# Performance work log

Hardware: AMD Instinct MI355X
Metric: run time of the kernel (lower is better)

Reference implementation:

```python
import jax, jax.numpy as jnp
import numpy as np

D_MODEL = 128
N_HEAD = 4
D_K = D_MODEL // N_HEAD
NEG = -1e30


def setup_inputs() -> dict:
    key = jax.random.key(0)
    ks = jax.random.split(key, 6)
    B, L = 8, 2048
    x = jax.random.normal(ks[0], (B, D_MODEL, L), dtype=jnp.float32)
    # mask: 1.0 = masked position (per mask_logits convention), 0.0 = keep
    mask = jax.random.randint(ks[1], (B, L), 0, 2).astype(jnp.float32)
    s = 1.0 / np.sqrt(D_MODEL)
    Wq = jax.random.normal(ks[2], (N_HEAD, D_MODEL, D_K), dtype=jnp.float32) * s
    Wk = jax.random.normal(ks[3], (N_HEAD, D_MODEL, D_K), dtype=jnp.float32) * s
    Wv = jax.random.normal(ks[4], (N_HEAD, D_MODEL, D_K), dtype=jnp.float32) * s
    Wo = jax.random.normal(ks[5], (D_MODEL, D_MODEL), dtype=jnp.float32) * s
    return {"x": x, "mask": mask, "Wq": Wq, "Wk": Wk, "Wv": Wv, "Wo": Wo}


def reference(x, mask, Wq, Wk, Wv, Wo):
    # x: [B, d_model, L] -> [B, L, d_model]
    xt = jnp.transpose(x, (0, 2, 1))
    # per-head projections, stacked over head axis: [B, H, L, d_k]
    q = jnp.einsum('bld,hdk->bhlk', xt, Wq)
    k = jnp.einsum('bld,hdk->bhlk', xt, Wk)
    v = jnp.einsum('bld,hdk->bhlk', xt, Wv)
    scale = 1.0 / jnp.sqrt(jnp.asarray(D_K, dtype=x.dtype))
    # scores: [B, H, Lq, Lk]
    scores = jnp.einsum('bhqd,bhkd->bhqk', q, k) * scale
    hmask = mask[:, None, None, :]  # additive pre-softmax mask over keys
    scores = scores * (1.0 - hmask) + hmask * NEG
    attn = jax.nn.softmax(scores, axis=-1)
    attn = attn * mask[:, None, :, None]  # multiplicative post-softmax mask over queries
    heads = jnp.einsum('bhqk,bhkd->bhqd', attn, v)  # [B, H, L, d_k]
    B, H, L, dk = heads.shape
    head = jnp.transpose(heads, (0, 2, 1, 3)).reshape(B, L, H * dk)  # concat heads
    out = head @ Wo  # [B, L, d_model]
    return jnp.transpose(out, (0, 2, 1))  # [B, d_model, L]
```

## Files before the change

kernel.cpp:

```cpp
#include <hip/hip_runtime.h>
#include <hip/hip_bf16.h>
#include <math.h>

#define BATCH 8
#define LSEQ 2048
#define DM 128
#define NH 4
#define DK 32

constexpr float SCALE = 0.17677669529663687f;
constexpr float LOG2E = 1.4426950408889634f;
constexpr float SL = SCALE * LOG2E;

typedef __attribute__((ext_vector_type(8))) __bf16 bf16x8;
typedef __attribute__((ext_vector_type(16))) float f32x16;
typedef __attribute__((ext_vector_type(2))) unsigned uint2v;

__device__ __forceinline__ bf16x8 as_bf16x8(uint4 u) {
    union { uint4 a; bf16x8 b; } c; c.a = u; return c.b;
}
__device__ __forceinline__ unsigned pack_bf2(float lo, float hi) {
    __hip_bfloat162 h = __float22bfloat162_rn(make_float2(lo, hi));
    union { __hip_bfloat162 a; unsigned b; } c; c.a = h; return c.b;
}
__device__ __forceinline__ unsigned short bf16u(float f) {
    union { __hip_bfloat16 h; unsigned short u; } c; c.h = __float2bfloat16(f); return c.u;
}

__global__ __launch_bounds__(256) void qkv_mfma_kernel(const float* __restrict__ x,
    const float* __restrict__ Wq, const float* __restrict__ Wk, const float* __restrict__ Wv,
    const float* __restrict__ mask,
    unsigned short* __restrict__ Qb, unsigned short* __restrict__ Kb,
    unsigned short* __restrict__ V4, int* __restrict__ cnt)
{
    const int b = blockIdx.x;
    const int which = blockIdx.y;
    const int lt = blockIdx.z;
    const int tid = threadIdx.x;
    const int wv = tid >> 6;
    const int lane = tid & 63;
    const int ql = lane & 31;
    const int hi = lane >> 5;
    const int l = lt * 64 + (wv & 1) * 32 + ql;
    const int hbase = (wv >> 1) * 2;

    __shared__ unsigned short wl[4][16][32][8];
    __shared__ int slotbuf[64];
    __shared__ int wsumI[4];

    const float* W = (which == 0 ? Wq : (which == 1 ? Wk : Wv));

    #pragma unroll
    for (int it = 0; it < 16; ++it) {
        const int flat = (it * 256 + tid) * 4;
        float4 v = *reinterpret_cast<const float4*>(W + flat);
        const int dk0 = flat & 31;
        const int d   = (flat >> 5) & 127;
        const int h   = flat >> 12;
        wl[h][d >> 3][dk0 + 0][d & 7] = bf16u(v.x);
        wl[h][d >> 3][dk0 + 1][d & 7] = bf16u(v.y);
        wl[h][d >> 3][dk0 + 2][d & 7] = bf16u(v.z);
        wl[h][d >> 3][dk0 + 3][d & 7] = bf16u(v.w);
    }

    if (which != 0) {
        const int nchunk = (lt + 1) * 8;
        int c = 0;
        if (tid < nchunk) {
            const float* mb = mask + (size_t)b * LSEQ + tid * 8;
            #pragma unroll
            for (int i = 0; i < 8; ++i) c += (mb[i] == 0.0f) ? 1 : 0;
        }
        int inc = c;
        #pragma unroll
        for (int off = 1; off < 64; off <<= 1) {
            int v = __shfl_up(inc, off);
            if (lane >= off) inc += v;
        }
        if (lane == 63) wsumI[wv] = inc;
        __syncthreads();
        int wpre = 0;
        #pragma unroll
        for (int wN = 0; wN < 4; ++wN) if (wN < wv) wpre += wsumI[wN];
        const int excl = wpre + inc - c;
        if (tid >= lt * 8 && tid < lt * 8 + 8) {
            const float* mb = mask + (size_t)b * LSEQ + tid * 8;
            int run = excl;
            #pragma unroll
            for (int i = 0; i < 8; ++i) {
                slotbuf[(tid - lt * 8) * 8 + i] = run;
                run += (mb[i] == 0.0f) ? 1 : 0;
            }
        }
        if (which == 1 && lt == 31 && tid == 255) cnt[b] = wpre + inc;
    }
    __syncthreads();

    const float* xcol = x + (size_t)b * DM * LSEQ + l;

    f32x16 acc0, acc1;
    #pragma unroll
    for (int r = 0; r < 16; ++r) { acc0[r] = 0.f; acc1[r] = 0.f; }

    #pragma unroll
    for (int d0 = 0; d0 < DM; d0 += 16) {
        const int dblk = (d0 >> 3) + hi;
        float xv[8];
        #pragma unroll
        for (int i = 0; i < 8; ++i) xv[i] = xcol[(size_t)(d0 + 8 * hi + i) * LSEQ];
        uint4 xp = make_uint4(pack_bf2(xv[0], xv[1]), pack_bf2(xv[2], xv[3]),
                              pack_bf2(xv[4], xv[5]), pack_bf2(xv[6], xv[7]));
        const bf16x8 xf = as_bf16x8(xp);
        uint4 wp0 = *reinterpret_cast<const uint4*>(&wl[hbase + 0][dblk][ql][0]);
        uint4 wp1 = *reinterpret_cast<const uint4*>(&wl[hbase + 1][dblk][ql][0]);
        acc0 = __builtin_amdgcn_mfma_f32_32x32x16_bf16(as_bf16x8(wp0), xf, acc0, 0, 0, 0);
        acc1 = __builtin_amdgcn_mfma_f32_32x32x16_bf16(as_bf16x8(wp1), xf, acc1, 0, 0, 0);
    }

    bool store = true;
    int slot = l;
    if (which != 0) {
        if (mask[(size_t)b * LSEQ + l] == 0.0f) slot = slotbuf[(wv & 1) * 32 + ql];
        else store = false;
    }
    if (store) {
        if (which < 2) {
            const float fold = (which == 0) ? SL : 1.0f;
            unsigned short* base0 = (which == 0 ? Qb : Kb);
            #pragma unroll
            for (int hh = 0; hh < 2; ++hh) {
                const f32x16& A = hh ? acc1 : acc0;
                const int bh = b * NH + hbase + hh;
                unsigned short* rowp = base0 + ((size_t)bh * LSEQ + slot) * DK;
                unsigned dw[8];
                #pragma unroll
                for (int j = 0; j < 8; ++j) dw[j] = pack_bf2(A[2*j] * fold, A[2*j+1] * fold);
                *reinterpret_cast<uint2*>(rowp + 4*hi)      = make_uint2(dw[0], dw[1]);
                *reinterpret_cast<uint2*>(rowp + 8 + 4*hi)  = make_uint2(dw[2], dw[3]);
                *reinterpret_cast<uint2*>(rowp + 16 + 4*hi) = make_uint2(dw[4], dw[5]);
                *reinterpret_cast<uint2*>(rowp + 24 + 4*hi) = make_uint2(dw[6], dw[7]);
            }
        } else {
            const int sbase = (slot >> 5) * 1024 + ((slot >> 4) & 1) * 512
                            + ((slot >> 3) & 1) * 256 + (slot & 7) + hi * 32;
            #pragma unroll
            for (int hh = 0; hh < 2; ++hh) {
                const f32x16& A = hh ? acc1 : acc0;
                const int bh = b * NH + hbase + hh;
                unsigned short* vb = V4 + (size_t)bh * (LSEQ * DK) + sbase;
                #pragma unroll
                for (int r = 0; r < 16; ++r)
                    vb[8 * (r & 3) + 64 * (r >> 2)] = bf16u(A[r]);
            }
        }
    }
}

__global__ __launch_bounds__(512, 4) void attnproj_kernel(
    const unsigned short* __restrict__ Qb, const unsigned short* __restrict__ Kb,
    const unsigned short* __restrict__ V4, const float* __restrict__ mask,
    const int* __restrict__ cnt, const float* __restrict__ Wo,
    float* __restrict__ out)
{
    const int b = blockIdx.x & 7;
    const int q0 = (blockIdx.x >> 3) * 32;
    const int tid = threadIdx.x;
    const int wid = tid >> 6;
    const int h = wid >> 1;
    const int kw = wid & 1;
    const int lane = tid & 63;
    const int ql = lane & 31;
    const int hi = lane >> 5;
    const int bh = b * NH + h;
    const int n = cnt[b];

    __shared__ __align__(16) char smem[17408];
    float* red = reinterpret_cast<float*>(smem);
    unsigned short* hd = reinterpret_cast<unsigned short*>(smem);

    const uint4* Qp = reinterpret_cast<const uint4*>(Qb + ((size_t)bh * LSEQ + q0 + ql) * DK);
    const bf16x8 qf0 = as_bf16x8(Qp[hi]);
    const bf16x8 qf1 = as_bf16x8(Qp[2 + hi]);

    const unsigned short* Kbase = Kb + (size_t)bh * LSEQ * DK;
    const unsigned short* Vb4   = V4 + (size_t)bh * LSEQ * DK;

    f32x16 acc;
    #pragma unroll
    for (int r = 0; r < 16; ++r) acc[r] = 0.f;
    f32x16 zero;
    #pragma unroll
    for (int r = 0; r < 16; ++r) zero[r] = 0.f;
    float la0 = 0.f, la1 = 0.f;

    auto ldk0 = [&](int k) { return reinterpret_cast<const uint4*>(Kbase + (size_t)(k + ql) * DK)[hi]; };
    auto ldk1 = [&](int k) { return reinterpret_cast<const uint4*>(Kbase + (size_t)(k + ql) * DK)[2 + hi]; };
    auto ldv0 = [&](int k) { return reinterpret_cast<const uint4*>(Vb4 + (size_t)(k >> 5) * 1024)[lane]; };
    auto ldv1 = [&](int k) { return reinterpret_cast<const uint4*>(Vb4 + (size_t)(k >> 5) * 1024)[64 + lane]; };

    auto compute = [&](uint4 kv0, uint4 kv1, uint4 vv0, uint4 vv1, int k0, bool pred) {
        f32x16 s = __builtin_amdgcn_mfma_f32_32x32x16_bf16(as_bf16x8(kv0), qf0, zero, 0, 0, 0);
        s = __builtin_amdgcn_mfma_f32_32x32x16_bf16(as_bf16x8(kv1), qf1, s, 0, 0, 0);
        unsigned w[8];
        #pragma unroll
        for (int j = 0; j < 8; ++j) {
            float e0 = exp2f(s[2*j]);
            float e1 = exp2f(s[2*j+1]);
            if (pred) {
                const int r0 = 2*j, r1 = 2*j + 1;
                if (k0 + (r0 & 3) + 8*(r0 >> 2) + 4*hi >= n) e0 = 0.f;
                if (k0 + (r1 & 3) + 8*(r1 >> 2) + 4*hi >= n) e1 = 0.f;
            }
            la0 += e0;
            la1 += e1;
            w[j] = pack_bf2(e0, e1);
        }
        uint2v p0 = __builtin_amdgcn_permlane32_swap(w[0], w[2], false, false);
        uint2v p1 = __builtin_amdgcn_permlane32_swap(w[1], w[3], false, false);
        uint2v p2 = __builtin_amdgcn_permlane32_swap(w[4], w[6], false, false);
        uint2v p3 = __builtin_amdgcn_permlane32_swap(w[5], w[7], false, false);
        uint4 b0 = make_uint4(p0[0], p1[0], p0[1], p1[1]);
        uint4 b1 = make_uint4(p2[0], p3[0], p2[1], p3[1]);
        acc = __builtin_amdgcn_mfma_f32_32x32x16_bf16(as_bf16x8(vv0), as_bf16x8(b0), acc, 0, 0, 0);
        acc = __builtin_amdgcn_mfma_f32_32x32x16_bf16(as_bf16x8(vv1), as_bf16x8(b1), acc, 0, 0, 0);
    };

    const int nfull = n & ~31;
    int k = kw * 32;
    if (k < nfull) {
        uint4 ka0 = ldk0(k), ka1 = ldk1(k), va0 = ldv0(k), va1 = ldv1(k);
        for (; k + 64 < nfull; k += 64) {
            uint4 kb0 = ldk0(k + 64), kb1 = ldk1(k + 64);
            uint4 vb0 = ldv0(k + 64), vb1 = ldv1(k + 64);
            compute(ka0, ka1, va0, va1, k, false);
            ka0 = kb0; ka1 = kb1; va0 = vb0; va1 = vb1;
        }
        compute(ka0, ka1, va0, va1, k, false);
    }
    if ((n & 31) && (((nfull >> 5) & 1) == kw)) {
        uint4 ka0 = ldk0(nfull), ka1 = ldk1(nfull);
        uint4 va0 = ldv0(nfull), va1 = ldv1(nfull);
        compute(ka0, ka1, va0, va1, nfull, true);
    }

    float la = la0 + la1;

    if (kw == 1) {
        float* r0 = red + ((size_t)h * 64 + lane) * 17;
        #pragma unroll
        for (int r = 0; r < 16; ++r) r0[r] = acc[r];
        r0[16] = la;
    }
    __syncthreads();
    float wgt = 0.f;
    if (kw == 0) {
        const float* r0 = red + ((size_t)h * 64 + lane) * 17;
        #pragma unroll
        for (int r = 0; r < 16; ++r) acc[r] += r0[r];
        la += r0[16];
        const float lf = la + __shfl_xor(la, 32);
        const float mq = mask[(size_t)b * LSEQ + q0 + ql];
        wgt = (lf > 0.f) ? (mq / lf) : 0.f;
    }
    __syncthreads();

    if (kw == 0) {
        unsigned short* hrow = hd + ql * 136 + h * DK + 4 * hi;
        #pragma unroll
        for (int g = 0; g < 4; ++g) {
            uint2 p = make_uint2(pack_bf2(acc[4*g+0]*wgt, acc[4*g+1]*wgt),
                                 pack_bf2(acc[4*g+2]*wgt, acc[4*g+3]*wgt));
            *reinterpret_cast<uint2*>(hrow + 8*g) = p;
        }
    }
    __syncthreads();

    if (wid < 4) {
        const int jq = wid;
        f32x16 pacc;
        #pragma unroll
        for (int r = 0; r < 16; ++r) pacc[r] = 0.f;
        #pragma unroll
        for (int ks = 0; ks < 8; ++ks) {
            const int k0 = ks * 16 + 8 * hi;
            uint4 bp = *reinterpret_cast<const uint4*>(hd + ql * 136 + k0);
            const float* wcol = Wo + (size_t)k0 * DM + jq * 32 + ql;
            float w[8];
            #pragma unroll
            for (int i = 0; i < 8; ++i) w[i] = wcol[(size_t)i * DM];
            uint4 ap = make_uint4(pack_bf2(w[0], w[1]), pack_bf2(w[2], w[3]),
                                  pack_bf2(w[4], w[5]), pack_bf2(w[6], w[7]));
            pacc = __builtin_amdgcn_mfma_f32_32x32x16_bf16(as_bf16x8(ap), as_bf16x8(bp), pacc, 0, 0, 0);
        }
        float* obase = out + (size_t)b * DM * LSEQ + q0 + ql;
        #pragma unroll
        for (int r = 0; r < 16; ++r) {
            const int j = jq * 32 + (r & 3) + 8 * (r >> 2) + 4 * hi;
            obase[(size_t)j * LSEQ] = pacc[r];
        }
    }
}

extern "C" void kernel_launch(void* const* d_in, const int* in_sizes, int n_in,
                              void* d_out, int out_size, void* d_ws, size_t ws_size,
                              hipStream_t stream)
{
    const float* x    = (const float*)d_in[0];
    const float* mask = (const float*)d_in[1];
    const float* Wq   = (const float*)d_in[2];
    const float* Wk   = (const float*)d_in[3];
    const float* Wv   = (const float*)d_in[4];
    const float* Wo   = (const float*)d_in[5];
    float* out = (float*)d_out;

    char* wsb = (char*)d_ws;
    const size_t NBF = (size_t)BATCH * NH * LSEQ * DK;
    unsigned short* Qb  = (unsigned short*)wsb;
    unsigned short* Kb  = Qb + NBF;
    unsigned short* V4  = Kb + NBF;
    int* cnt  = (int*)(wsb + 24ull * 1024 * 1024);

    qkv_mfma_kernel<<<dim3(BATCH, 3, LSEQ / 64), dim3(256), 0, stream>>>(
        x, Wq, Wk, Wv, mask, Qb, Kb, V4, cnt);
    attnproj_kernel<<<dim3(BATCH * LSEQ / 32), dim3(512), 0, stream>>>(
        Qb, Kb, V4, mask, cnt, Wo, out);
}
```

Baseline: 43.35 us.

## Compact masked-out queries and skip attention for them

The QKV kernel now also compacts query rows, storing only queries whose post-softmax mask is nonzero, and records scatter index lists for kept and dropped positions. The attention kernel processes only the compacted queries; blocks past the kept count just write zeros to the dropped output columns. This removes attention and projection work for query rows that the multiplicative mask zeroes anyway. In exchange, output stores become scattered through index lists, there is extra index-list traffic, and the saving depends on how many queries the mask drops.

After: 42.32 us. 2.4% less time.

```diff
diff --git a/kernel.cpp b/kernel.cpp
--- a/kernel.cpp
+++ b/kernel.cpp
@@ -31,7 +31,8 @@
     const float* __restrict__ Wq, const float* __restrict__ Wk, const float* __restrict__ Wv,
     const float* __restrict__ mask,
     unsigned short* __restrict__ Qb, unsigned short* __restrict__ Kb,
-    unsigned short* __restrict__ V4, int* __restrict__ cnt)
+    unsigned short* __restrict__ V4, int* __restrict__ cnt,
+    int* __restrict__ qpos1, int* __restrict__ qpos0)
 {
     const int b = blockIdx.x;
     const int which = blockIdx.y;
@@ -63,7 +64,7 @@
         wl[h][d >> 3][dk0 + 3][d & 7] = bf16u(v.w);
     }
 
-    if (which != 0) {
+    {
         const int nchunk = (lt + 1) * 8;
         int c = 0;
         if (tid < nchunk) {
@@ -95,6 +96,13 @@
         if (which == 1 && lt == 31 && tid == 255) cnt[b] = wpre + inc;
     }
     __syncthreads();
+
+    if (which == 1 && tid < 64) {
+        const int l64 = lt * 64 + tid;
+        const int s = slotbuf[tid];
+        if (mask[(size_t)b * LSEQ + l64] == 0.0f) qpos0[b * LSEQ + s] = l64;
+        else                                      qpos1[b * LSEQ + (l64 - s)] = l64;
+    }
 
     const float* xcol = x + (size_t)b * DM * LSEQ + l;
 
@@ -117,12 +125,12 @@
         acc1 = __builtin_amdgcn_mfma_f32_32x32x16_bf16(as_bf16x8(wp1), xf, acc1, 0, 0, 0);
     }
 
-    bool store = true;
-    int slot = l;
-    if (which != 0) {
-        if (mask[(size_t)b * LSEQ + l] == 0.0f) slot = slotbuf[(wv & 1) * 32 + ql];
-        else store = false;
-    }
+    const float mv = mask[(size_t)b * LSEQ + l];
+    const int zb = slotbuf[(wv & 1) * 32 + ql];
+    bool store;
+    int slot;
+    if (which == 0) { store = (mv != 0.0f); slot = l - zb; }
+    else            { store = (mv == 0.0f); slot = zb; }
     if (store) {
         if (which < 2) {
             const float fold = (which == 0) ? SL : 1.0f;
@@ -158,8 +166,9 @@
 
 __global__ __launch_bounds__(512, 4) void attnproj_kernel(
     const unsigned short* __restrict__ Qb, const unsigned short* __restrict__ Kb,
-    const unsigned short* __restrict__ V4, const float* __restrict__ mask,
-    const int* __restrict__ cnt, const float* __restrict__ Wo,
+    const unsigned short* __restrict__ V4,
+    const int* __restrict__ cnt, const int* __restrict__ qpos1,
+    const int* __restrict__ qpos0, const float* __restrict__ Wo,
     float* __restrict__ out)
 {
     const int b = blockIdx.x & 7;
@@ -173,6 +182,21 @@
     const int hi = lane >> 5;
     const int bh = b * NH + h;
     const int n = cnt[b];
+    const int nq = LSEQ - n;
+
+    if (q0 >= nq) {
+        if (wid < 4) {
+            const int jq = wid;
+            const int pos = qpos0[b * LSEQ + (q0 + ql - nq)];
+            float* obase = out + (size_t)b * DM * LSEQ + pos;
+            #pragma unroll
+            for (int r = 0; r < 16; ++r) {
+                const int j = jq * 32 + (r & 3) + 8 * (r >> 2) + 4 * hi;
+                obase[(size_t)j * LSEQ] = 0.f;
+            }
+        }
+        return;
+    }
 
     __shared__ __align__(16) char smem[17408];
     float* red = reinterpret_cast<float*>(smem);
@@ -259,8 +283,7 @@
         for (int r = 0; r < 16; ++r) acc[r] += r0[r];
         la += r0[16];
         const float lf = la + __shfl_xor(la, 32);
-        const float mq = mask[(size_t)b * LSEQ + q0 + ql];
-        wgt = (lf > 0.f) ? (mq / lf) : 0.f;
+        wgt = (lf > 0.f) ? (1.0f / lf) : 0.f;
     }
     __syncthreads();
 
@@ -292,11 +315,14 @@
                                   pack_bf2(w[4], w[5]), pack_bf2(w[6], w[7]));
             pacc = __builtin_amdgcn_mfma_f32_32x32x16_bf16(as_bf16x8(ap), as_bf16x8(bp), pacc, 0, 0, 0);
         }
-        float* obase = out + (size_t)b * DM * LSEQ + q0 + ql;
+        const int i = q0 + ql;
+        const bool valid = (i < nq);
+        const int pos = valid ? qpos1[b * LSEQ + i] : qpos0[b * LSEQ + (i - nq)];
+        float* obase = out + (size_t)b * DM * LSEQ + pos;
         #pragma unroll
         for (int r = 0; r < 16; ++r) {
             const int j = jq * 32 + (r & 3) + 8 * (r >> 2) + 4 * hi;
-            obase[(size_t)j * LSEQ] = pacc[r];
+            obase[(size_t)j * LSEQ] = valid ? pacc[r] : 0.f;
         }
     }
 }
@@ -318,10 +344,12 @@
     unsigned short* Qb  = (unsigned short*)wsb;
     unsigned short* Kb  = Qb + NBF;
     unsigned short* V4  = Kb + NBF;
-    int* cnt  = (int*)(wsb + 24ull * 1024 * 1024);
+    int* cnt   = (int*)(wsb + 24ull * 1024 * 1024);
+    int* qpos1 = (int*)(wsb + 24ull * 1024 * 1024 + 4096);
+    int* qpos0 = qpos1 + (size_t)BATCH * LSEQ;
 
     qkv_mfma_kernel<<<dim3(BATCH, 3, LSEQ / 64), dim3(256), 0, stream>>>(
-        x, Wq, Wk, Wv, mask, Qb, Kb, V4, cnt);
+        x, Wq, Wk, Wv, mask, Qb, Kb, V4, cnt, qpos1, qpos0);
     attnproj_kernel<<<dim3(BATCH * LSEQ / 32), dim3(512), 0, stream>>>(
-        Qb, Kb, V4, mask, cnt, Wo, out);
-}
+        Qb, Kb, V4, cnt, qpos1, qpos0, Wo, out);
+}
```
